# Kernel tuning notes

Hardware: AMD Instinct MI355X
Metric: run time of the kernel (lower is better)

## Reference

```python
import jax, jax.numpy as jnp
import numpy as np

B, S, D, H = 2, 2048, 1024, 16
HD = D // H
SPARSITY = 0.1
LAMBDA_MAX = 10.0
ALPHA = 5.0


def local_prior_mask(seq_len: int, sparsity: float) -> jnp.ndarray:
    # |i - j| <= window_size // 2, window_size = int(seq_len * sparsity)
    window_size = max(1, int(seq_len * sparsity))
    rows = jnp.arange(seq_len)[:, None]
    cols = jnp.arange(seq_len)[None, :]
    return jnp.abs(rows - cols) <= (window_size // 2)


def setup_inputs() -> dict:
    key = jax.random.key(0)
    ks = jax.random.split(key, 12)
    scale = 1.0 / np.sqrt(D)
    inp = {
        'x': jax.random.normal(ks[0], (B, S, D), dtype=jnp.float32),
        'u_prev': jax.random.uniform(ks[1], (B, 1), dtype=jnp.float32),
        'Wq': jax.random.normal(ks[2], (D, D), dtype=jnp.float32) * scale,
        'bq': jnp.zeros((D,), dtype=jnp.float32),
        'Wk': jax.random.normal(ks[3], (D, D), dtype=jnp.float32) * scale,
        'bk': jnp.zeros((D,), dtype=jnp.float32),
        'Wv': jax.random.normal(ks[4], (D, D), dtype=jnp.float32) * scale,
        'bv': jnp.zeros((D,), dtype=jnp.float32),
        'Wo': jax.random.normal(ks[5], (D, D), dtype=jnp.float32) * scale,
        'bo': jnp.zeros((D,), dtype=jnp.float32),
    }
    return inp


def reference(x, u_prev, Wq, bq, Wk, bk, Wv, bv, Wo, bo):
    b, s, _ = x.shape
    # projections (torch Linear: y = x W^T + b)
    def proj(W, bias):
        return (x @ W.T + bias).reshape(b, s, H, HD).transpose(0, 2, 1, 3)  # [B,H,S,HD]
    q = proj(Wq, bq)
    k = proj(Wk, bk)
    v = proj(Wv, bv)

    # dynamic gating: lambda = lambda_max * exp(-alpha * u_prev), shape [B,1,1,1]
    lam = (LAMBDA_MAX * jnp.exp(-ALPHA * u_prev)).reshape(b, 1, 1, 1)

    prior = local_prior_mask(s, SPARSITY)  # [S,S] bool

    scores = jnp.einsum('bhqd,bhkd->bhqk', q, k) / jnp.sqrt(jnp.asarray(HD, x.dtype))
    # additive prior bias: penalize positions outside the structural prior by -lambda
    scores = scores - lam * (~prior).astype(x.dtype)

    attn = jax.nn.softmax(scores, axis=-1)
    out = jnp.einsum('bhqk,bhkd->bhqd', attn, v)           # [B,H,S,HD]
    out = out.transpose(0, 2, 1, 3).reshape(b, s, D)        # [B,S,D]
    out = out @ Wo.T + bo
    return out, lam.reshape(b, 1)
```

## Files before the change

### kernel.cpp

```cpp
#include <hip/hip_runtime.h>

typedef __attribute__((ext_vector_type(8))) short short8;
typedef __attribute__((ext_vector_type(4))) float f32x4;

#define MFMA16(a,b,c) __builtin_amdgcn_mfma_f32_16x16x32_bf16(a,b,c,0,0,0)

__device__ __forceinline__ unsigned short f2bf(float f){
  unsigned int u = __float_as_uint(f);
  u += 0x7FFF + ((u>>16)&1);
  return (unsigned short)(u>>16);
}

__device__ __forceinline__ void gl_lds16(const void* g, void* l){
  __builtin_amdgcn_global_load_lds((const __attribute__((address_space(1))) void*)g,
                                   (__attribute__((address_space(3))) void*)l, 16, 0, 0);
}

__global__ void cvt_bf16(const float* __restrict__ src, unsigned short* __restrict__ dst, int n){
  int i = (blockIdx.x*blockDim.x + threadIdx.x)*4;
  if (i + 3 < n){
    float4 v = *(const float4*)(src + i);
    ushort4 o;
    o.x = f2bf(v.x); o.y = f2bf(v.y); o.z = f2bf(v.z); o.w = f2bf(v.w);
    *(ushort4*)(dst + i) = o;
  }
}

template<int MODE>
__global__ __launch_bounds__(256) void gemm_bt(
  const unsigned short* __restrict__ A,
  const unsigned short* __restrict__ Bw,
  const float* __restrict__ bias0, const float* __restrict__ bias1, const float* __restrict__ bias2,
  unsigned short* __restrict__ Qo, unsigned short* __restrict__ Ko, unsigned short* __restrict__ VTo,
  float* __restrict__ Co,
  int M, int N, int K)
{
  __shared__ unsigned short As[2][128*32];
  __shared__ unsigned short Bs[2][128*32];
  const int tid = threadIdx.x;
  const int m0 = blockIdx.y*128, n0 = blockIdx.x*128;
  const int w = tid>>6, lane = tid&63, lr = lane&15, lg = lane>>4;
  const int wm = w>>1, wn = w&1;
  const int nk = K/32;

  auto stage = [&](int buf, int kt){
    const unsigned short* Ag = A + (size_t)m0*K + kt*32;
    const unsigned short* Bg = Bw + (size_t)n0*K + kt*32;
    #pragma unroll
    for (int it=0; it<2; ++it){
      int slot = it*256 + tid;
      gl_lds16(Ag + (size_t)(slot>>2)*K + (slot&3)*8, &As[buf][slot*8]);
    }
    #pragma unroll
    for (int it=0; it<2; ++it){
      int slot = it*256 + tid;
      gl_lds16(Bg + (size_t)(slot>>2)*K + (slot&3)*8, &Bs[buf][slot*8]);
    }
  };

  f32x4 acc[4][4] = {};
  stage(0,0);
  for (int kt=0; kt<nk; ++kt){
    int cur = kt&1;
    __syncthreads();
    if (kt+1 < nk) stage(cur^1, kt+1);
    short8 af[4], bfr[4];
    #pragma unroll
    for (int i=0;i<4;++i) af[i]  = *(const short8*)&As[cur][(wm*64 + i*16 + lr)*32 + lg*8];
    #pragma unroll
    for (int j=0;j<4;++j) bfr[j] = *(const short8*)&Bs[cur][(wn*64 + j*16 + lr)*32 + lg*8];
    #pragma unroll
    for (int i=0;i<4;++i)
      #pragma unroll
      for (int j=0;j<4;++j)
        acc[i][j] = MFMA16(af[i], bfr[j], acc[i][j]);
  }

  #pragma unroll
  for (int i=0;i<4;++i){
    #pragma unroll
    for (int j=0;j<4;++j){
      const int n  = n0 + wn*64 + j*16 + lr;
      const int mb = m0 + wm*64 + i*16 + lg*4;
      if (MODE==0){
        const int which = n>>10, nn = n&1023;
        const float bv = (which==0) ? bias0[nn] : (which==1) ? bias1[nn] : bias2[nn];
        const int h = nn>>6, hd = nn&63;
        #pragma unroll
        for (int r=0;r<4;++r){
          const int m = mb + r;
          const int b = m>>11, s = m&2047;
          const unsigned short u = f2bf(acc[i][j][r] + bv);
          const size_t bh = (size_t)(b*16 + h);
          if (which==0)      Qo[(bh*2048 + s)*64 + hd] = u;
          else if (which==1) Ko[(bh*2048 + s)*64 + hd] = u;
          else               VTo[(bh*64 + hd)*2048 + s] = u;
        }
      } else {
        const float bv = bias0[n];
        #pragma unroll
        for (int r=0;r<4;++r){
          const int m = mb + r;
          Co[(size_t)m*N + n] = acc[i][j][r] + bv;
        }
      }
    }
  }
}

__global__ __launch_bounds__(256, 4) void attn_k(
  const unsigned short* __restrict__ Qb,
  const unsigned short* __restrict__ Kb,
  const unsigned short* __restrict__ VT,
  const float* __restrict__ u_prev,
  unsigned short* __restrict__ Out)
{
  const int qt = blockIdx.x, bh = blockIdx.y;
  const int b = bh>>4, h = bh&15;
  const float lam = 10.f * __expf(-5.f * u_prev[b]);
  const int tid = threadIdx.x;
  const int w = tid>>6, lane = tid&63, lr = lane&15, lg = lane>>4;
  const int q0 = qt*64 + w*16;

  const unsigned short* Qp = Qb + (size_t)bh*2048*64;
  const unsigned short* Kp = Kb + (size_t)bh*2048*64;
  const unsigned short* Vp = VT + (size_t)bh*64*2048;

  __shared__ unsigned short Ks[2][2048];
  __shared__ unsigned short Vs[2][2048];
  __shared__ unsigned short p_lds[4][16][32];

  const int ks2 = tid>>7, krow = (tid>>2)&31, kseg = tid&3;
  const int vrow = tid>>2, vseg = tid&3;

  auto stage = [&](int buf, int kt){
    const int k0 = kt*32;
    gl_lds16(Kp + (size_t)(k0+krow)*64 + ks2*32 + kseg*8, &Ks[buf][tid*8]);
    gl_lds16(Vp + (size_t)vrow*2048 + k0 + vseg*8,        &Vs[buf][tid*8]);
  };

  short8 qf0 = *(const short8*)&Qp[(size_t)(q0+lr)*64 +      lg*8];
  short8 qf1 = *(const short8*)&Qp[(size_t)(q0+lr)*64 + 32 + lg*8];

  float l_run[4] = {0.f, 0.f, 0.f, 0.f};
  f32x4 o0 = {}, o1 = {}, o2 = {}, o3 = {};

  stage(0, 0);
  for (int kt=0; kt<64; ++kt){
    const int cur = kt&1;
    __syncthreads();
    if (kt+1 < 64) stage(cur^1, kt+1);

    const unsigned short* Kc = Ks[cur];
    const unsigned short* Vc = Vs[cur];
    short8 k00 = *(const short8*)&Kc[        (     lr)*32 + lg*8];
    short8 k01 = *(const short8*)&Kc[1024 + (     lr)*32 + lg*8];
    short8 k10 = *(const short8*)&Kc[        (16 + lr)*32 + lg*8];
    short8 k11 = *(const short8*)&Kc[1024 + (16 + lr)*32 + lg*8];
    short8 vf0 = *(const short8*)&Vc[(     lr)*32 + lg*8];
    short8 vf1 = *(const short8*)&Vc[(16 + lr)*32 + lg*8];
    short8 vf2 = *(const short8*)&Vc[(32 + lr)*32 + lg*8];
    short8 vf3 = *(const short8*)&Vc[(48 + lr)*32 + lg*8];

    f32x4 s0 = {}, s1 = {};
    s0 = MFMA16(qf0, k00, s0); s0 = MFMA16(qf1, k01, s0);
    s1 = MFMA16(qf0, k10, s1); s1 = MFMA16(qf1, k11, s1);

    const int k0_ = kt*32;
    const int cls_ = (k0_ > q0 + 117 || k0_ < q0 - 133) ? 2
                   : (k0_ >= q0 - 87 && k0_ <= q0 + 71) ? 0 : 1;
    #pragma unroll
    for (int r=0;r<4;++r){
      const int qi_ = q0 + lg*4 + r;
      float v0 = s0[r]*0.125f, v1 = s1[r]*0.125f;
      if (cls_ == 2){ v0 -= lam; v1 -= lam; }
      else if (cls_ == 1){
        int d0 = qi_ - (k0_ + lr);      if (d0<0) d0 = -d0;
        int d1 = qi_ - (k0_ + 16 + lr); if (d1<0) d1 = -d1;
        if (d0 > 102) v0 -= lam;
        if (d1 > 102) v1 -= lam;
      }
      const float p0 = __expf(v0), p1 = __expf(v1);
      l_run[r] += p0 + p1;
      p_lds[w][lg*4+r][lr]      = f2bf(p0);
      p_lds[w][lg*4+r][16 + lr] = f2bf(p1);
    }
    short8 pa = *(const short8*)&p_lds[w][lr][lg*8];
    o0 = MFMA16(pa, vf0, o0);
    o1 = MFMA16(pa, vf1, o1);
    o2 = MFMA16(pa, vf2, o2);
    o3 = MFMA16(pa, vf3, o3);
  }

  #pragma unroll
  for (int off=1; off<16; off<<=1)
    #pragma unroll
    for (int r=0;r<4;++r)
      l_run[r] += __shfl_xor(l_run[r], off, 64);

  #pragma unroll
  for (int r=0;r<4;++r){
    const int qi = q0 + lg*4 + r;
    const float linv = 1.0f / l_run[r];
    unsigned short* op = &Out[((size_t)b*2048 + qi)*1024 + h*64 + lr];
    op[0]  = f2bf(o0[r] * linv);
    op[16] = f2bf(o1[r] * linv);
    op[32] = f2bf(o2[r] * linv);
    op[48] = f2bf(o3[r] * linv);
  }
}

__global__ void tail_k(const float* __restrict__ u, float* __restrict__ out){
  int i = threadIdx.x;
  if (i < 2) out[4194304 + i] = 10.f*__expf(-5.f*u[i]);
}

extern "C" void kernel_launch(void* const* d_in, const int* in_sizes, int n_in,
                              void* d_out, int out_size, void* d_ws, size_t ws_size,
                              hipStream_t stream){
  const float* x  = (const float*)d_in[0];
  const float* u  = (const float*)d_in[1];
  const float* Wq = (const float*)d_in[2];
  const float* bq = (const float*)d_in[3];
  const float* Wk = (const float*)d_in[4];
  const float* bk = (const float*)d_in[5];
  const float* Wv = (const float*)d_in[6];
  const float* bv = (const float*)d_in[7];
  const float* Wo = (const float*)d_in[8];
  const float* bo = (const float*)d_in[9];
  float* out = (float*)d_out;

  unsigned char* ws = (unsigned char*)d_ws;
  unsigned short* xb    = (unsigned short*)(ws);
  unsigned short* attnb = xb;
  unsigned short* Wqkvb = (unsigned short*)(ws + 8388608);
  unsigned short* Wob   = (unsigned short*)(ws + 14680064);
  unsigned short* Qb2   = (unsigned short*)(ws + 16777216);
  unsigned short* Kb2   = (unsigned short*)(ws + 25165824);
  unsigned short* VTb   = (unsigned short*)(ws + 33554432);

  cvt_bf16<<<4096, 256, 0, stream>>>(x,  xb, 4194304);
  cvt_bf16<<<1024, 256, 0, stream>>>(Wq, Wqkvb,            1048576);
  cvt_bf16<<<1024, 256, 0, stream>>>(Wk, Wqkvb + 1048576,  1048576);
  cvt_bf16<<<1024, 256, 0, stream>>>(Wv, Wqkvb + 2097152,  1048576);
  cvt_bf16<<<1024, 256, 0, stream>>>(Wo, Wob, 1048576);

  gemm_bt<0><<<dim3(24,32), 256, 0, stream>>>(xb, Wqkvb, bq, bk, bv,
                                              Qb2, Kb2, VTb, nullptr, 4096, 3072, 1024);
  attn_k<<<dim3(32,32), 256, 0, stream>>>(Qb2, Kb2, VTb, u, attnb);
  gemm_bt<1><<<dim3(8,32), 256, 0, stream>>>(attnb, Wob, bo, nullptr, nullptr,
                                             nullptr, nullptr, nullptr, out, 4096, 1024, 1024);
  tail_k<<<1, 64, 0, stream>>>(u, out);
}
```

Before: 167.9 us.

## Reorder K/V LDS staging layout, pad P tile, use exp2 with folded scale

```diff
diff --git a/kernel.cpp b/kernel.cpp
--- a/kernel.cpp
+++ b/kernel.cpp
@@ -9,6 +9,14 @@
   unsigned int u = __float_as_uint(f);
   u += 0x7FFF + ((u>>16)&1);
   return (unsigned short)(u>>16);
+}
+
+__device__ __forceinline__ float fexp2(float x){
+#if __has_builtin(__builtin_amdgcn_exp2f)
+  return __builtin_amdgcn_exp2f(x);
+#else
+  return exp2f(x);
+#endif
 }
 
 __device__ __forceinline__ void gl_lds16(const void* g, void* l){
@@ -118,6 +126,7 @@
   const int qt = blockIdx.x, bh = blockIdx.y;
   const int b = bh>>4, h = bh&15;
   const float lam = 10.f * __expf(-5.f * u_prev[b]);
+  const float nlamb = -lam * 1.4426950408889634f;
   const int tid = threadIdx.x;
   const int w = tid>>6, lane = tid&63, lr = lane&15, lg = lane>>4;
   const int q0 = qt*64 + w*16;
@@ -128,19 +137,18 @@
 
   __shared__ unsigned short Ks[2][2048];
   __shared__ unsigned short Vs[2][2048];
-  __shared__ unsigned short p_lds[4][16][32];
-
-  const int ks2 = tid>>7, krow = (tid>>2)&31, kseg = tid&3;
-  const int vrow = tid>>2, vseg = tid&3;
+  __shared__ unsigned short p_lds[4][16][40];
 
   auto stage = [&](int buf, int kt){
     const int k0 = kt*32;
-    gl_lds16(Kp + (size_t)(k0+krow)*64 + ks2*32 + kseg*8, &Ks[buf][tid*8]);
-    gl_lds16(Vp + (size_t)vrow*2048 + k0 + vseg*8,        &Vs[buf][tid*8]);
+    gl_lds16(Kp + (size_t)(k0 + (tid&31))*64 + (tid>>5)*8, &Ks[buf][tid*8]);
+    gl_lds16(Vp + (size_t)(tid&63)*2048 + k0 + (tid>>6)*8, &Vs[buf][tid*8]);
   };
 
   short8 qf0 = *(const short8*)&Qp[(size_t)(q0+lr)*64 +      lg*8];
   short8 qf1 = *(const short8*)&Qp[(size_t)(q0+lr)*64 + 32 + lg*8];
+
+  const float c1 = 0.18033688011112042f;
 
   float l_run[4] = {0.f, 0.f, 0.f, 0.f};
   f32x4 o0 = {}, o1 = {}, o2 = {}, o3 = {};
@@ -153,14 +161,14 @@
 
     const unsigned short* Kc = Ks[cur];
     const unsigned short* Vc = Vs[cur];
-    short8 k00 = *(const short8*)&Kc[        (     lr)*32 + lg*8];
-    short8 k01 = *(const short8*)&Kc[1024 + (     lr)*32 + lg*8];
-    short8 k10 = *(const short8*)&Kc[        (16 + lr)*32 + lg*8];
-    short8 k11 = *(const short8*)&Kc[1024 + (16 + lr)*32 + lg*8];
-    short8 vf0 = *(const short8*)&Vc[(     lr)*32 + lg*8];
-    short8 vf1 = *(const short8*)&Vc[(16 + lr)*32 + lg*8];
-    short8 vf2 = *(const short8*)&Vc[(32 + lr)*32 + lg*8];
-    short8 vf3 = *(const short8*)&Vc[(48 + lr)*32 + lg*8];
+    short8 k00 = *(const short8*)&Kc[(lg*32 +      lr)*8];
+    short8 k01 = *(const short8*)&Kc[1024 + (lg*32 +      lr)*8];
+    short8 k10 = *(const short8*)&Kc[(lg*32 + 16 + lr)*8];
+    short8 k11 = *(const short8*)&Kc[1024 + (lg*32 + 16 + lr)*8];
+    short8 vf0 = *(const short8*)&Vc[(lg*64 +      lr)*8];
+    short8 vf1 = *(const short8*)&Vc[(lg*64 + 16 + lr)*8];
+    short8 vf2 = *(const short8*)&Vc[(lg*64 + 32 + lr)*8];
+    short8 vf3 = *(const short8*)&Vc[(lg*64 + 48 + lr)*8];
 
     f32x4 s0 = {}, s1 = {};
     s0 = MFMA16(qf0, k00, s0); s0 = MFMA16(qf1, k01, s0);
@@ -172,15 +180,16 @@
     #pragma unroll
     for (int r=0;r<4;++r){
       const int qi_ = q0 + lg*4 + r;
-      float v0 = s0[r]*0.125f, v1 = s1[r]*0.125f;
-      if (cls_ == 2){ v0 -= lam; v1 -= lam; }
+      float b0 = 0.f, b1 = 0.f;
+      if (cls_ == 2){ b0 = nlamb; b1 = nlamb; }
       else if (cls_ == 1){
         int d0 = qi_ - (k0_ + lr);      if (d0<0) d0 = -d0;
         int d1 = qi_ - (k0_ + 16 + lr); if (d1<0) d1 = -d1;
-        if (d0 > 102) v0 -= lam;
-        if (d1 > 102) v1 -= lam;
+        if (d0 > 102) b0 = nlamb;
+        if (d1 > 102) b1 = nlamb;
       }
-      const float p0 = __expf(v0), p1 = __expf(v1);
+      const float p0 = fexp2(fmaf(s0[r], c1, b0));
+      const float p1 = fexp2(fmaf(s1[r], c1, b1));
       l_run[r] += p0 + p1;
       p_lds[w][lg*4+r][lr]      = f2bf(p0);
       p_lds[w][lg*4+r][16 + lr] = f2bf(p1);
```

Result: no change. 166.6 us (-0.8%).
